# Kernel optimization log

Measured on AMD Instinct MI355X. Metric: run time of the kernel, lower is better.

## Reference

```python
import jax, jax.numpy as jnp
import numpy as np

MAX_DIM = 1024
VOCAB = 257
DEPTH = 6
Q_DIM = MAX_DIM // 4  # 256
EXP_DIMS = [1, 2, 4, 8, 16, 32, 64, 128]  # expander sizes: current_q doubles up to Q_DIM
BATCH, SEQ = 8, 4096


def qlinear(q, W):
    """Quaternion Hamilton-product linear.
    q: [..., in, 4] (last dim = r,i,j,k components), W: [4, out, in] (stacked r,i,j,k weights).
    Returns [..., out, 4].
    """
    # P[..., o, w, a] = F.linear(component_a, W_w)  -> all 16 small GEMMs in one einsum
    P = jnp.einsum('...ia,woi->...owa', q, W)
    Pr, Pi, Pj, Pk = P[..., 0, :], P[..., 1, :], P[..., 2, :], P[..., 3, :]  # each [..., out, 4]
    out_r = Pr[..., 0] - Pi[..., 1] - Pj[..., 2] - Pk[..., 3]
    out_i = Pi[..., 0] + Pr[..., 1] + Pk[..., 2] - Pj[..., 3]
    out_j = Pj[..., 0] - Pk[..., 1] + Pr[..., 2] + Pi[..., 3]
    out_k = Pk[..., 0] + Pj[..., 1] - Pi[..., 2] + Pr[..., 3]
    return jnp.stack([out_r, out_i, out_j, out_k], axis=-1)


def qnormalize(q):
    norm = jnp.linalg.norm(q, axis=-1, keepdims=True)
    return q / (norm + 1e-8)


def setup_inputs() -> dict:
    key = jax.random.key(0)
    ks = jax.random.split(key, 4 + len(EXP_DIMS))
    inp = {}
    inp['x'] = jax.random.randint(ks[0], (BATCH, SEQ), 0, VOCAB)
    inp['emb'] = jax.random.normal(ks[1], (VOCAB, 4), dtype=jnp.float32)
    for idx, cq in enumerate(EXP_DIMS):
        scale = cq ** (-0.5)
        inp[f'w_exp{idx}'] = jax.random.uniform(ks[2 + idx], (4, cq, cq), jnp.float32, -scale, scale)
    scale = Q_DIM ** (-0.5)
    inp['w_layers'] = jax.random.uniform(ks[-2], (DEPTH, 4, Q_DIM, Q_DIM), jnp.float32, -scale, scale)
    inp['w_head'] = jax.random.normal(ks[-1], (VOCAB, MAX_DIM), dtype=jnp.float32) * MAX_DIM ** (-0.5)
    return inp


def reference(x, emb, w_exp0, w_exp1, w_exp2, w_exp3, w_exp4, w_exp5, w_exp6, w_exp7,
              w_layers, w_head):
    q = emb[x][:, :, None, :]  # [B, S, 1, 4]
    for w in (w_exp0, w_exp1, w_exp2, w_exp3, w_exp4, w_exp5, w_exp6, w_exp7):
        delta = jnp.tanh(qlinear(q, w))
        q = jnp.concatenate([q + delta, q - delta], axis=2)  # doubles quaternion dim
    for d in range(DEPTH):
        q = qnormalize(qlinear(q, w_layers[d]))
    stability_loss = jnp.mean(jnp.abs(q[..., 0]))
    h_flat = q.reshape(x.shape[0], x.shape[1], -1)  # [B, S, MAX_DIM]
    logits = jnp.einsum('bsd,vd->bsv', h_flat, w_head)
    return (logits, stability_loss)
```

## Files before the change

### kernel.cpp

```cpp
#include <hip/hip_runtime.h>


typedef _Float16 f16x8 __attribute__((ext_vector_type(8)));
typedef float    f32x4 __attribute__((ext_vector_type(4)));

#define GL2LDS16(gp, lp) __builtin_amdgcn_global_load_lds(                     \
    (const __attribute__((address_space(1))) void*)(gp),                       \
    (__attribute__((address_space(3))) void*)(lp), 16, 0, 0)

__device__ __forceinline__ unsigned short f2h(float f) {
  union { _Float16 h; unsigned short u; } c;
  c.h = (_Float16)f;
  return c.u;
}
__device__ __forceinline__ float h2f(unsigned short u) {
  union { unsigned short u; _Float16 h; } c;
  c.u = u;
  return (float)c.h;
}

__global__ __launch_bounds__(256) void expand_ham(
    const float* __restrict__ w, unsigned short* __restrict__ out,
    int cq, int kbits, int total) {
  int id = blockIdx.x * 256 + threadIdx.x;
  if (id >= total) return;
  const int K = 1 << kbits;
  const int n = id >> kbits;
  const int k = id & (K - 1);
  float val = 0.f;
  if (n < 4 * cq) {
    const int o = n >> 2, a = n & 3, i = k >> 2, b = k & 3;
    const int   comp[4][4] = {{0,1,2,3},{1,0,3,2},{2,3,0,1},{3,2,1,0}};
    const float sgn [4][4] = {{1.f,-1.f,-1.f,-1.f},{1.f,1.f,1.f,-1.f},
                              {1.f,-1.f,1.f,1.f},{1.f,1.f,-1.f,1.f}};
    val = sgn[a][b] * w[comp[a][b] * cq * cq + o * cq + i];
  }
  out[id] = f2h(val);
}

__global__ __launch_bounds__(256) void conv_head(
    const float* __restrict__ wh, unsigned short* __restrict__ out) {
  int id = blockIdx.x * 256 + threadIdx.x;
  int v = id >> 10, k = id & 1023;
  out[id] = f2h(v < 257 ? wh[v * 1024 + k] : 0.f);
}

template <int CQ>
__device__ __forceinline__ void exp_step(float (&q)[16][4],
                                         const float* __restrict__ w) {
  float d[CQ][4];
#pragma unroll
  for (int o = 0; o < CQ; o++) {
    float pr = 0.f, pi = 0.f, pj = 0.f, pk = 0.f;
#pragma unroll
    for (int i = 0; i < CQ; i++) {
      const float wr = w[0 * CQ * CQ + o * CQ + i];
      const float wi = w[1 * CQ * CQ + o * CQ + i];
      const float wj = w[2 * CQ * CQ + o * CQ + i];
      const float wk = w[3 * CQ * CQ + o * CQ + i];
      const float qr = q[i][0], qi = q[i][1], qj = q[i][2], qk = q[i][3];
      pr += wr * qr - wi * qi - wj * qj - wk * qk;
      pi += wi * qr + wr * qi + wk * qj - wj * qk;
      pj += wj * qr - wk * qi + wr * qj + wi * qk;
      pk += wk * qr + wj * qi - wi * qj + wr * qk;
    }
    d[o][0] = tanhf(pr); d[o][1] = tanhf(pi);
    d[o][2] = tanhf(pj); d[o][3] = tanhf(pk);
  }
#pragma unroll
  for (int o = 0; o < CQ; o++)
#pragma unroll
    for (int a = 0; a < 4; a++) {
      const float dd = d[o][a], qq = q[o][a];
      q[o][a]      = qq + dd;
      q[CQ + o][a] = qq - dd;
    }
}

__global__ __launch_bounds__(256) void embed_expand(
    const int* __restrict__ x, const float* __restrict__ emb,
    const float* __restrict__ w0, const float* __restrict__ w1,
    const float* __restrict__ w2, const float* __restrict__ w3,
    unsigned short* __restrict__ out) {
  const int t = blockIdx.x * 256 + threadIdx.x;
  float q[16][4];
  const int v = x[t];
  const float4 e = *(const float4*)(emb + v * 4);
  q[0][0] = e.x; q[0][1] = e.y; q[0][2] = e.z; q[0][3] = e.w;
  exp_step<1>(q, w0);
  exp_step<2>(q, w1);
  exp_step<4>(q, w2);
  exp_step<8>(q, w3);
  ushort4* o4 = (ushort4*)(out + (size_t)t * 64);
#pragma unroll
  for (int c = 0; c < 16; c++) {
    ushort4 u;
    u.x = f2h(q[c][0]); u.y = f2h(q[c][1]);
    u.z = f2h(q[c][2]); u.w = f2h(q[c][3]);
    o4[c] = u;
  }
}

template <int EPI>
__global__ __launch_bounds__(256) void gemm_epi(
    const unsigned short* __restrict__ W,
    const unsigned short* __restrict__ Act,
    unsigned short* __restrict__ OutB, float* __restrict__ OutF,
    int K, int Nreal, int ldout) {
  __shared__ unsigned short Wt[128 * 32];
  __shared__ unsigned short At[128 * 32];
  __shared__ float lsum[4];

  const int tid  = threadIdx.x;
  const int wave = tid >> 6;
  const int lane = tid & 63;
  const int l15  = lane & 15;
  const int quad = lane >> 4;
  const int mblock = blockIdx.x * 128;
  const int nblock = blockIdx.y * 128;
  const int wn = (wave & 1) * 64;
  const int wm = (wave >> 1) * 64;

  f32x4 acc[4][4];
  const f32x4 zero = {0.f, 0.f, 0.f, 0.f};
#pragma unroll
  for (int a = 0; a < 4; a++)
#pragma unroll
    for (int b = 0; b < 4; b++) acc[a][b] = zero;

  const int row0 = tid >> 2;
  const int sub  = tid & 3;
  const unsigned short* gW0 = W   + (size_t)(nblock + row0)      * K + sub * 8;
  const unsigned short* gW1 = W   + (size_t)(nblock + row0 + 64) * K + sub * 8;
  const unsigned short* gA0 = Act + (size_t)(mblock + row0)      * K + sub * 8;
  const unsigned short* gA1 = Act + (size_t)(mblock + row0 + 64) * K + sub * 8;
  unsigned short* lW0 = &Wt[(wave * 64) * 8];
  unsigned short* lW1 = &Wt[(256 + wave * 64) * 8];
  unsigned short* lA0 = &At[(wave * 64) * 8];
  unsigned short* lA1 = &At[(256 + wave * 64) * 8];

  for (int kb = 0; kb < K; kb += 32) {
    GL2LDS16(gW0 + kb, lW0);
    GL2LDS16(gW1 + kb, lW1);
    GL2LDS16(gA0 + kb, lA0);
    GL2LDS16(gA1 + kb, lA1);
    __syncthreads();

    f16x8 afr[4], bfr[4];
#pragma unroll
    for (int tn = 0; tn < 4; tn++)
      afr[tn] = *(const f16x8*)&Wt[(wn + tn * 16 + l15) * 32 + quad * 8];
#pragma unroll
    for (int tm = 0; tm < 4; tm++)
      bfr[tm] = *(const f16x8*)&At[(wm + tm * 16 + l15) * 32 + quad * 8];
#pragma unroll
    for (int tn = 0; tn < 4; tn++)
#pragma unroll
      for (int tm = 0; tm < 4; tm++)
        acc[tn][tm] = __builtin_amdgcn_mfma_f32_16x16x32_f16(
            afr[tn], bfr[tm], acc[tn][tm], 0, 0, 0);
    __syncthreads();
  }

  if constexpr (EPI == 0) {
#pragma unroll
    for (int tn = 0; tn < 4; tn++) {
      const int n = nblock + wn + tn * 16 + quad * 4;
      if (n < Nreal) {
#pragma unroll
        for (int tm = 0; tm < 4; tm++) {
          const int token = mblock + wm + tm * 16 + l15;
          const f32x4 v = acc[tn][tm];
          const unsigned short* ip = Act + (size_t)token * K + n;
          const float i0 = h2f(ip[0]), i1 = h2f(ip[1]);
          const float i2 = h2f(ip[2]), i3 = h2f(ip[3]);
          const float d0 = tanhf(v[0]), d1 = tanhf(v[1]);
          const float d2 = tanhf(v[2]), d3 = tanhf(v[3]);
          ushort4 up, um;
          up.x = f2h(i0 + d0); up.y = f2h(i1 + d1);
          up.z = f2h(i2 + d2); up.w = f2h(i3 + d3);
          um.x = f2h(i0 - d0); um.y = f2h(i1 - d1);
          um.z = f2h(i2 - d2); um.w = f2h(i3 - d3);
          *(ushort4*)&OutB[(size_t)token * ldout + n] = up;
          *(ushort4*)&OutB[(size_t)token * ldout + Nreal + n] = um;
        }
      }
    }
  } else if constexpr (EPI == 1 || EPI == 2) {
    float loss = 0.f;
#pragma unroll
    for (int tn = 0; tn < 4; tn++) {
      const int n = nblock + wn + tn * 16 + quad * 4;
#pragma unroll
      for (int tm = 0; tm < 4; tm++) {
        const int token = mblock + wm + tm * 16 + l15;
        const f32x4 v = acc[tn][tm];
        const float nrm =
            sqrtf(v[0] * v[0] + v[1] * v[1] + v[2] * v[2] + v[3] * v[3]);
        const float inv = 1.f / (nrm + 1e-8f);
        ushort4 u;
        u.x = f2h(v[0] * inv); u.y = f2h(v[1] * inv);
        u.z = f2h(v[2] * inv); u.w = f2h(v[3] * inv);
        *(ushort4*)&OutB[(size_t)token * ldout + n] = u;
        if constexpr (EPI == 2) loss += fabsf(v[0] * inv);
      }
    }
    if constexpr (EPI == 2) {
#pragma unroll
      for (int off = 32; off > 0; off >>= 1) loss += __shfl_down(loss, off);
      if (lane == 0) lsum[wave] = loss;
      __syncthreads();
      if (tid == 0)
        atomicAdd(OutF,
                  (lsum[0] + lsum[1] + lsum[2] + lsum[3]) * (1.f / 8388608.f));
    }
  } else {
#pragma unroll
    for (int tn = 0; tn < 4; tn++) {
      const int n = nblock + wn + tn * 16 + quad * 4;
      if (n < 257) {
#pragma unroll
        for (int tm = 0; tm < 4; tm++) {
          const int token = mblock + wm + tm * 16 + l15;
          const f32x4 v = acc[tn][tm];
#pragma unroll
          for (int r = 0; r < 4; r++)
            if (n + r < 257) OutF[(size_t)token * 257 + n + r] = v[r];
        }
      }
    }
  }
}

extern "C" void kernel_launch(void* const* d_in, const int* in_sizes, int n_in,
                              void* d_out, int out_size, void* d_ws,
                              size_t ws_size, hipStream_t stream) {
  const int*   x    = (const int*)d_in[0];
  const float* emb  = (const float*)d_in[1];
  const float* we0  = (const float*)d_in[2];
  const float* we1  = (const float*)d_in[3];
  const float* we2  = (const float*)d_in[4];
  const float* we3  = (const float*)d_in[5];
  const float* we4  = (const float*)d_in[6];
  const float* we5  = (const float*)d_in[7];
  const float* we6  = (const float*)d_in[8];
  const float* we7  = (const float*)d_in[9];
  const float* wlay = (const float*)d_in[10];
  const float* wh   = (const float*)d_in[11];
  float* out = (float*)d_out;

  char* p = (char*)d_ws;
  auto alloc = [&](size_t bytes) {
    void* r = (void*)p;
    p += (bytes + 255) & ~(size_t)255;
    return r;
  };
  unsigned short* act0 = (unsigned short*)alloc(32768ull * 1024 * 2);
  unsigned short* act1 = (unsigned short*)alloc(32768ull * 1024 * 2);
  unsigned short* E4 = (unsigned short*)alloc(128 * 64 * 2);
  unsigned short* E5 = (unsigned short*)alloc(128 * 128 * 2);
  unsigned short* E6 = (unsigned short*)alloc(256 * 256 * 2);
  unsigned short* E7 = (unsigned short*)alloc(512 * 512 * 2);
  unsigned short* EL = (unsigned short*)alloc(6ull * 1024 * 1024 * 2);
  unsigned short* WH = (unsigned short*)alloc(384 * 1024 * 2);

  hipMemsetAsync(out + 8421376, 0, 4, stream);

  expand_ham<<<dim3(8192 / 256), 256, 0, stream>>>(we4, E4, 16, 6, 128 * 64);
  expand_ham<<<dim3(16384 / 256), 256, 0, stream>>>(we5, E5, 32, 7, 128 * 128);
  expand_ham<<<dim3(65536 / 256), 256, 0, stream>>>(we6, E6, 64, 8, 256 * 256);
  expand_ham<<<dim3(262144 / 256), 256, 0, stream>>>(we7, E7, 128, 9,
                                                     512 * 512);
  for (int d = 0; d < 6; d++)
    expand_ham<<<dim3(1048576 / 256), 256, 0, stream>>>(
        wlay + (size_t)d * 262144, EL + (size_t)d * 1048576, 256, 10, 1048576);
  conv_head<<<dim3(384 * 1024 / 256), 256, 0, stream>>>(wh, WH);

  embed_expand<<<dim3(128), 256, 0, stream>>>(x, emb, we0, we1, we2, we3, act0);

  gemm_epi<0><<<dim3(256, 1), 256, 0, stream>>>(E4, act0, act1, nullptr, 64,
                                                64, 128);
  gemm_epi<0><<<dim3(256, 1), 256, 0, stream>>>(E5, act1, act0, nullptr, 128,
                                                128, 256);
  gemm_epi<0><<<dim3(256, 2), 256, 0, stream>>>(E6, act0, act1, nullptr, 256,
                                                256, 512);
  gemm_epi<0><<<dim3(256, 4), 256, 0, stream>>>(E7, act1, act0, nullptr, 512,
                                                512, 1024);

  unsigned short* a = act0;
  unsigned short* b = act1;
  for (int d = 0; d < 5; d++) {
    gemm_epi<1><<<dim3(256, 8), 256, 0, stream>>>(EL + (size_t)d * 1048576, a,
                                                  b, nullptr, 1024, 1024, 1024);
    unsigned short* t = a; a = b; b = t;
  }
  gemm_epi<2><<<dim3(256, 8), 256, 0, stream>>>(EL + 5ull * 1048576, a, b,
                                                out + 8421376, 1024, 1024,
                                                1024);
  { unsigned short* t = a; a = b; b = t; }

  gemm_epi<3><<<dim3(256, 3), 256, 0, stream>>>(WH, a, nullptr, out, 1024, 257,
                                                0);
}
```

Before: 982.5 us.

## Double K-step per barrier and swap grid axes so N tiles share activation rows

Each main-loop iteration of the GEMM now loads two 32-wide K slabs into separate LDS buffers and runs both MFMA batches before syncing. This halves the number of barrier pairs per tile. The block grid is also transposed so the N tiles of one activation row-block sit next to each other in launch order, which should improve L2 reuse of the activation tile. LDS use doubles, which may lower occupancy. The K=64 expander GEMM still divides evenly.

```diff
diff --git a/kernel.cpp b/kernel.cpp
--- a/kernel.cpp
+++ b/kernel.cpp
@@ -107,8 +107,10 @@
     const unsigned short* __restrict__ Act,
     unsigned short* __restrict__ OutB, float* __restrict__ OutF,
     int K, int Nreal, int ldout) {
-  __shared__ unsigned short Wt[128 * 32];
-  __shared__ unsigned short At[128 * 32];
+  __shared__ unsigned short WtL[128 * 32];
+  __shared__ unsigned short WtH[128 * 32];
+  __shared__ unsigned short AtL[128 * 32];
+  __shared__ unsigned short AtH[128 * 32];
   __shared__ float lsum[4];
 
   const int tid  = threadIdx.x;
@@ -116,8 +118,8 @@
   const int lane = tid & 63;
   const int l15  = lane & 15;
   const int quad = lane >> 4;
-  const int mblock = blockIdx.x * 128;
-  const int nblock = blockIdx.y * 128;
+  const int nblock = blockIdx.x * 128;
+  const int mblock = blockIdx.y * 128;
   const int wn = (wave & 1) * 64;
   const int wm = (wave >> 1) * 64;
 
@@ -134,31 +136,56 @@
   const unsigned short* gW1 = W   + (size_t)(nblock + row0 + 64) * K + sub * 8;
   const unsigned short* gA0 = Act + (size_t)(mblock + row0)      * K + sub * 8;
   const unsigned short* gA1 = Act + (size_t)(mblock + row0 + 64) * K + sub * 8;
-  unsigned short* lW0 = &Wt[(wave * 64) * 8];
-  unsigned short* lW1 = &Wt[(256 + wave * 64) * 8];
-  unsigned short* lA0 = &At[(wave * 64) * 8];
-  unsigned short* lA1 = &At[(256 + wave * 64) * 8];
-
-  for (int kb = 0; kb < K; kb += 32) {
-    GL2LDS16(gW0 + kb, lW0);
-    GL2LDS16(gW1 + kb, lW1);
-    GL2LDS16(gA0 + kb, lA0);
-    GL2LDS16(gA1 + kb, lA1);
+  unsigned short* lWL0 = &WtL[wave * 512];
+  unsigned short* lWL1 = &WtL[2048 + wave * 512];
+  unsigned short* lWH0 = &WtH[wave * 512];
+  unsigned short* lWH1 = &WtH[2048 + wave * 512];
+  unsigned short* lAL0 = &AtL[wave * 512];
+  unsigned short* lAL1 = &AtL[2048 + wave * 512];
+  unsigned short* lAH0 = &AtH[wave * 512];
+  unsigned short* lAH1 = &AtH[2048 + wave * 512];
+
+  for (int kb = 0; kb < K; kb += 64) {
+    GL2LDS16(gW0 + kb,      lWL0);
+    GL2LDS16(gW1 + kb,      lWL1);
+    GL2LDS16(gW0 + kb + 32, lWH0);
+    GL2LDS16(gW1 + kb + 32, lWH1);
+    GL2LDS16(gA0 + kb,      lAL0);
+    GL2LDS16(gA1 + kb,      lAL1);
+    GL2LDS16(gA0 + kb + 32, lAH0);
+    GL2LDS16(gA1 + kb + 32, lAH1);
     __syncthreads();
 
-    f16x8 afr[4], bfr[4];
-#pragma unroll
-    for (int tn = 0; tn < 4; tn++)
-      afr[tn] = *(const f16x8*)&Wt[(wn + tn * 16 + l15) * 32 + quad * 8];
-#pragma unroll
-    for (int tm = 0; tm < 4; tm++)
-      bfr[tm] = *(const f16x8*)&At[(wm + tm * 16 + l15) * 32 + quad * 8];
-#pragma unroll
-    for (int tn = 0; tn < 4; tn++)
+    {
+      f16x8 afr[4], bfr[4];
+#pragma unroll
+      for (int tn = 0; tn < 4; tn++)
+        afr[tn] = *(const f16x8*)&WtL[(wn + tn * 16 + l15) * 32 + quad * 8];
 #pragma unroll
       for (int tm = 0; tm < 4; tm++)
-        acc[tn][tm] = __builtin_amdgcn_mfma_f32_16x16x32_f16(
-            afr[tn], bfr[tm], acc[tn][tm], 0, 0, 0);
+        bfr[tm] = *(const f16x8*)&AtL[(wm + tm * 16 + l15) * 32 + quad * 8];
+#pragma unroll
+      for (int tn = 0; tn < 4; tn++)
+#pragma unroll
+        for (int tm = 0; tm < 4; tm++)
+          acc[tn][tm] = __builtin_amdgcn_mfma_f32_16x16x32_f16(
+              afr[tn], bfr[tm], acc[tn][tm], 0, 0, 0);
+    }
+    {
+      f16x8 afr[4], bfr[4];
+#pragma unroll
+      for (int tn = 0; tn < 4; tn++)
+        afr[tn] = *(const f16x8*)&WtH[(wn + tn * 16 + l15) * 32 + quad * 8];
+#pragma unroll
+      for (int tm = 0; tm < 4; tm++)
+        bfr[tm] = *(const f16x8*)&AtH[(wm + tm * 16 + l15) * 32 + quad * 8];
+#pragma unroll
+      for (int tn = 0; tn < 4; tn++)
+#pragma unroll
+        for (int tm = 0; tm < 4; tm++)
+          acc[tn][tm] = __builtin_amdgcn_mfma_f32_16x16x32_f16(
+              afr[tn], bfr[tm], acc[tn][tm], 0, 0, 0);
+    }
     __syncthreads();
   }
 
@@ -278,27 +305,27 @@
 
   embed_expand<<<dim3(128), 256, 0, stream>>>(x, emb, we0, we1, we2, we3, act0);
 
-  gemm_epi<0><<<dim3(256, 1), 256, 0, stream>>>(E4, act0, act1, nullptr, 64,
+  gemm_epi<0><<<dim3(1, 256), 256, 0, stream>>>(E4, act0, act1, nullptr, 64,
                                                 64, 128);
-  gemm_epi<0><<<dim3(256, 1), 256, 0, stream>>>(E5, act1, act0, nullptr, 128,
+  gemm_epi<0><<<dim3(1, 256), 256, 0, stream>>>(E5, act1, act0, nullptr, 128,
                                                 128, 256);
-  gemm_epi<0><<<dim3(256, 2), 256, 0, stream>>>(E6, act0, act1, nullptr, 256,
+  gemm_epi<0><<<dim3(2, 256), 256, 0, stream>>>(E6, act0, act1, nullptr, 256,
                                                 256, 512);
-  gemm_epi<0><<<dim3(256, 4), 256, 0, stream>>>(E7, act1, act0, nullptr, 512,
+  gemm_epi<0><<<dim3(4, 256), 256, 0, stream>>>(E7, act1, act0, nullptr, 512,
                                                 512, 1024);
 
   unsigned short* a = act0;
   unsigned short* b = act1;
   for (int d = 0; d < 5; d++) {
-    gemm_epi<1><<<dim3(256, 8), 256, 0, stream>>>(EL + (size_t)d * 1048576, a,
+    gemm_epi<1><<<dim3(8, 256), 256, 0, stream>>>(EL + (size_t)d * 1048576, a,
                                                   b, nullptr, 1024, 1024, 1024);
     unsigned short* t = a; a = b; b = t;
   }
-  gemm_epi<2><<<dim3(256, 8), 256, 0, stream>>>(EL + 5ull * 1048576, a, b,
+  gemm_epi<2><<<dim3(8, 256), 256, 0, stream>>>(EL + 5ull * 1048576, a, b,
                                                 out + 8421376, 1024, 1024,
                                                 1024);
   { unsigned short* t = a; a = b; b = t; }
 
-  gemm_epi<3><<<dim3(256, 3), 256, 0, stream>>>(WH, a, nullptr, out, 1024, 257,
+  gemm_epi<3><<<dim3(3, 256), 256, 0, stream>>>(WH, a, nullptr, out, 1024, 257,
                                                 0);
 }
```

After: 879.0 us. -10.5%, faster.
